# Performance work log

Hardware: AMD Instinct MI355X
Metric: run time of the kernel (lower is better)

## Reference

```python
import jax, jax.numpy as jnp
import numpy as np

N = 100000
E = 1600000
IN_C, HID, OUT_C = 128, 256, 32
EPS = 1e-5
NEG_SLOPE = 0.1


def _leaky(x):
    return jnp.where(x >= 0, x, NEG_SLOPE * x)


def _gcn_conv(x, src, dst, ew, W, b, n):
    # x: [n, Fin] -> [n, Fout]; PyG GCNConv: add self-loops (weight 1),
    # symmetric normalization D^-1/2 (A+I) D^-1/2, then linear + bias.
    h = x @ W                                   # [n, Fout]
    loop = jnp.arange(n)
    src_f = jnp.concatenate([src, loop])        # [E+n]
    dst_f = jnp.concatenate([dst, loop])
    ew_f = jnp.concatenate([ew, jnp.ones((n,), x.dtype)])
    deg = jax.ops.segment_sum(ew_f, dst_f, num_segments=n)
    dinv = jnp.where(deg > 0, jax.lax.rsqrt(jnp.maximum(deg, EPS * 0 + 1e-12)), 0.0)
    norm = dinv[src_f] * ew_f * dinv[dst_f]     # [E+n]
    msg = h[src_f] * norm[:, None]              # gather + scale, [E+n, Fout]
    out = jax.ops.segment_sum(msg, dst_f, num_segments=n)
    return out + b


def _bn(x, gamma, beta):
    # training-mode BatchNorm1d over the node dimension
    m = x.mean(axis=0)
    v = x.var(axis=0)
    return (x - m) * jax.lax.rsqrt(v + EPS) * gamma + beta


def setup_inputs() -> dict:
    key = jax.random.key(0)
    ks = jax.random.split(key, 12)
    x = jax.random.normal(ks[0], (N, IN_C), dtype=jnp.float32)
    edge_index = jax.random.randint(ks[1], (2, E), 0, N, dtype=jnp.int64)
    edge_weight = jax.random.uniform(ks[2], (E,), dtype=jnp.float32)

    def lin(k, fi, fo):
        s = 1.0 / np.sqrt(fi)
        k1, k2 = jax.random.split(k)
        W = jax.random.uniform(k1, (fi, fo), jnp.float32, -s, s)
        b = jax.random.uniform(k2, (fo,), jnp.float32, -s, s)
        return W, b

    W1, b1 = lin(ks[3], IN_C, HID)
    W2, b2 = lin(ks[4], HID, HID)
    W3, b3 = lin(ks[5], HID, HID)
    Wl1, bl1 = lin(ks[6], HID, HID)
    Wl2, bl2 = lin(ks[7], HID, OUT_C)
    ones = jnp.ones((HID,), jnp.float32)
    zeros = jnp.zeros((HID,), jnp.float32)
    return {
        "x": x, "edge_index": edge_index, "edge_weight": edge_weight,
        "W1": W1, "b1": b1, "g1": ones, "be1": zeros,
        "W2": W2, "b2": b2, "g2": ones, "be2": zeros,
        "W3": W3, "b3": b3, "g3": ones, "be3": zeros,
        "Wl1": Wl1, "bl1": bl1, "Wl2": Wl2, "bl2": bl2,
    }


def reference(x, edge_index, edge_weight,
              W1, b1, g1, be1,
              W2, b2, g2, be2,
              W3, b3, g3, be3,
              Wl1, bl1, Wl2, bl2):
    src, dst = edge_index[0], edge_index[1]
    h = _gcn_conv(x, src, dst, edge_weight, W1, b1, N)
    h = _leaky(_bn(h, g1, be1))  # dropout = identity (eval)
    h = _gcn_conv(h, src, dst, edge_weight, W2, b2, N)
    h = _leaky(_bn(h, g2, be2))
    h = _gcn_conv(h, src, dst, edge_weight, W3, b3, N)
    h = _leaky(_bn(h, g3, be3))
    h = _leaky(h @ Wl1 + bl1)
    return h @ Wl2 + bl2
```

## Files before the change

kernel.cpp:

```cpp
#include <hip/hip_runtime.h>

#define NN 100000
#define NE 1600000
#define EPS_BN 1e-5f
#define NSHADOW 64
#define STATS_SC_OFF (NSHADOW*512)
#define STATS_SH_OFF (NSHADOW*512 + 256)

typedef unsigned short ushort_t;
typedef unsigned long long u64;
typedef _Float16 f16;
typedef short v8s __attribute__((ext_vector_type(8)));
typedef float v4f __attribute__((ext_vector_type(4)));
typedef f16 f16x2 __attribute__((ext_vector_type(2)));
typedef f16 f16x4 __attribute__((ext_vector_type(4)));

__device__ __forceinline__ float lk(float x){ return x >= 0.f ? x : 0.1f*x; }

__device__ __forceinline__ ushort_t f2bf(float x){
  unsigned u = __float_as_uint(x);
  unsigned r = (u + 0x7fffu + ((u >> 16) & 1u)) >> 16;
  return (ushort_t)r;
}
__device__ __forceinline__ float bf2f(ushort_t h){
  return __uint_as_float(((unsigned)h) << 16);
}
__device__ __forceinline__ void split2(float x, ushort_t& hi, ushort_t& lo){
  hi = f2bf(x);
  lo = f2bf(x - bf2f(hi));
}

__device__ __forceinline__ void gload16(const ushort_t* g, ushort_t* l){
  __builtin_amdgcn_global_load_lds((const __attribute__((address_space(1))) void*)g,
                                   (__attribute__((address_space(3))) void*)l, 16, 0, 0);
}

__global__ void zero_acc(u64* __restrict__ acc, int n){
  int i = blockIdx.x*256 + threadIdx.x;
  if (i < n) acc[i] = 0ull;
}

__global__ void edge_hist(const int* __restrict__ dst, const float* __restrict__ ew,
                          u64* __restrict__ acc, ushort_t* __restrict__ rank, int e){
  int i = blockIdx.x*256 + threadIdx.x;
  if (i < e){
    int d = dst[i];
    unsigned fx = (unsigned)(ew[i] * 67108864.0f + 0.5f);
    u64 old = atomicAdd(&acc[d], (1ull << 40) | (u64)fx);
    rank[i] = (ushort_t)(old >> 40);
  }
}

__global__ void finalize_acc(const u64* __restrict__ acc, float* __restrict__ dinv,
                             int* __restrict__ cnt, int n){
  int i = blockIdx.x*256 + threadIdx.x;
  if (i < n){
    u64 v = acc[i];
    cnt[i] = (int)(v >> 40);
    double w = (double)(v & 0xFFFFFFFFFFull) * (1.0/67108864.0);
    dinv[i] = rsqrtf((float)(1.0 + w));
  }
}

__global__ __launch_bounds__(1024) void scan_block(const int* __restrict__ in, int* __restrict__ out,
                                                   int* __restrict__ bsum, int n){
  __shared__ int s[1024];
  int t = threadIdx.x;
  int i = blockIdx.x*1024 + t;
  int v = (i < n) ? in[i] : 0;
  s[t] = v; __syncthreads();
  for (int off = 1; off < 1024; off <<= 1){
    int x = (t >= off) ? s[t-off] : 0;
    __syncthreads();
    s[t] += x;
    __syncthreads();
  }
  if (i < n) out[i] = s[t] - v;
  if (t == 1023) bsum[blockIdx.x] = s[1023];
}

__global__ void scan_small(int* __restrict__ bsum, int nb){
  __shared__ int s[128];
  int t = threadIdx.x;
  int v = (t < nb) ? bsum[t] : 0;
  s[t] = v; __syncthreads();
  for (int off = 1; off < 128; off <<= 1){
    int x = (t >= off) ? s[t-off] : 0;
    __syncthreads();
    s[t] += x;
    __syncthreads();
  }
  if (t < nb) bsum[t] = s[t] - v;
}

__global__ __launch_bounds__(1024) void scan_add(int* __restrict__ rp,
                                                 const int* __restrict__ bsum, int n, int etot){
  int i = blockIdx.x*1024 + threadIdx.x;
  if (i < n) rp[i] += bsum[blockIdx.x];
  if (i == 0) rp[n] = etot;
}

__global__ void fill_csr_k(const int* __restrict__ src, const int* __restrict__ dst,
                           const float* __restrict__ ew, const float* __restrict__ dinv,
                           const int* __restrict__ rp, const ushort_t* __restrict__ rank,
                           int2* __restrict__ csr_sw, int e){
  int i = blockIdx.x*256 + threadIdx.x;
  if (i >= e) return;
  int s = src[i], d = dst[i];
  int pos = rp[d] + (int)rank[i];
  float w = dinv[s] * ew[i] * dinv[d];
  csr_sw[pos] = make_int2(s, __float_as_int(w));
}

__global__ void cvt_x(const float* __restrict__ in, f16* __restrict__ out, int n4){
  int i = blockIdx.x*256 + threadIdx.x;
  if (i >= n4) return;
  float4 v = ((const float4*)in)[i];
  f16x4 h = (f16x4){(f16)v.x, (f16)v.y, (f16)v.z, (f16)v.w};
  ((f16x4*)out)[i] = h;
}

__global__ __launch_bounds__(256) void spmm16(const f16* __restrict__ h,
    const int* __restrict__ rp, const int2* __restrict__ csr_sw,
    const float* __restrict__ dinv, const float* __restrict__ bias,
    float* __restrict__ out, float* __restrict__ stats, int n){
  int nbase = __builtin_amdgcn_readfirstlane(blockIdx.x*16 + (threadIdx.x >> 6)*4);
  if (nbase >= n) return;
  int lane = threadIdx.x & 63;
  const f16* hb = h + lane*4;

  int P[5];
#pragma unroll
  for (int i = 0; i < 5; ++i) P[i] = __builtin_amdgcn_readfirstlane(rp[nbase+i]);
  int nchE[4];
#pragma unroll
  for (int jj = 0; jj < 4; ++jj){
    int nc = (P[jj+1] - P[jj] + 7) >> 3;
    nc = (nc + 1) & ~1;
    nchE[jj] = nc < 2 ? 2 : nc;
  }
  float di0 = dinv[nbase+0], di1 = dinv[nbase+1], di2 = dinv[nbase+2], di3 = dinv[nbase+3];
  f16x4 hv0 = *(const f16x4*)(hb + (size_t)(nbase+0)*256);
  f16x4 hv1 = *(const f16x4*)(hb + (size_t)(nbase+1)*256);
  f16x4 hv2 = *(const f16x4*)(hb + (size_t)(nbase+2)*256);
  f16x4 hv3 = *(const f16x4*)(hb + (size_t)(nbase+3)*256);
  float4 bb = *(const float4*)(bias + lane*4);

  float wA[8], wB[8];
  f16x4 vA[8], vB[8];
  float ax0, ay0, az0, aw0, ax1, ay1, az1, aw1;
  float ssx = 0.f, ssy = 0.f, ssz = 0.f, ssw = 0.f;
  float sqx = 0.f, sqy = 0.f, sqz = 0.f, sqw = 0.f;

#define LOADCH(W, V, BASE, PEND) do { \
    int2 _e[8]; \
    int _b = (BASE); int _pe = (PEND); \
    _Pragma("unroll") \
    for (int _i = 0; _i < 8; ++_i){ \
      int _pc = _b + _i; \
      _pc = _pc < _pe-1 ? _pc : _pe-1; \
      _pc = _pc > 0 ? _pc : 0; \
      _e[_i] = csr_sw[_pc]; \
    } \
    _Pragma("unroll") \
    for (int _i = 0; _i < 8; ++_i){ \
      W[_i] = (_b + _i < _pe) ? __int_as_float(_e[_i].y) : 0.f; \
      V[_i] = *(const f16x4*)(hb + (size_t)_e[_i].x*256); \
    } \
  } while(0)

#define FMACH(W, V) do { \
    _Pragma("unroll") \
    for (int _i = 0; _i < 8; _i += 2){ \
      ax0 = fmaf(W[_i],   (float)V[_i][0],   ax0); \
      ay0 = fmaf(W[_i],   (float)V[_i][1],   ay0); \
      az0 = fmaf(W[_i],   (float)V[_i][2],   az0); \
      aw0 = fmaf(W[_i],   (float)V[_i][3],   aw0); \
      ax1 = fmaf(W[_i+1], (float)V[_i+1][0], ax1); \
      ay1 = fmaf(W[_i+1], (float)V[_i+1][1], ay1); \
      az1 = fmaf(W[_i+1], (float)V[_i+1][2], az1); \
      aw1 = fmaf(W[_i+1], (float)V[_i+1][3], aw1); \
    } \
  } while(0)

#define NODE(jj, DI, HV, PRE) do { \
    const int p0_ = P[jj], pend_ = P[(jj)+1]; \
    const int ncE_ = nchE[jj]; \
    float c0_ = (DI)*(DI); \
    ax0 = fmaf(c0_, (float)(HV)[0], bb.x); \
    ay0 = fmaf(c0_, (float)(HV)[1], bb.y); \
    az0 = fmaf(c0_, (float)(HV)[2], bb.z); \
    aw0 = fmaf(c0_, (float)(HV)[3], bb.w); \
    ax1 = 0.f; ay1 = 0.f; az1 = 0.f; aw1 = 0.f; \
    int base_ = p0_ + 8; \
    for (int k_ = 0; k_ + 2 < ncE_; k_ += 2){ \
      LOADCH(wB, vB, base_, pend_); base_ += 8; \
      FMACH(wA, vA); \
      LOADCH(wA, vA, base_, pend_); base_ += 8; \
      FMACH(wB, vB); \
    } \
    LOADCH(wB, vB, base_, pend_); \
    FMACH(wA, vA); \
    PRE; \
    FMACH(wB, vB); \
    { \
      float fx_ = ax0+ax1, fy_ = ay0+ay1, fz_ = az0+az1, fw_ = aw0+aw1; \
      *(float4*)(out + (size_t)(nbase+(jj))*256 + lane*4) = \
          make_float4(fx_, fy_, fz_, fw_); \
      ssx += fx_; sqx = fmaf(fx_, fx_, sqx); \
      ssy += fy_; sqy = fmaf(fy_, fy_, sqy); \
      ssz += fz_; sqz = fmaf(fz_, fz_, sqz); \
      ssw += fw_; sqw = fmaf(fw_, fw_, sqw); \
    } \
  } while(0)

  LOADCH(wA, vA, P[0], P[1]);
  NODE(0, di0, hv0, LOADCH(wA, vA, P[1], P[2]));
  NODE(1, di1, hv1, LOADCH(wA, vA, P[2], P[3]));
  NODE(2, di2, hv2, LOADCH(wA, vA, P[3], P[4]));
  NODE(3, di3, hv3, (void)0);
#undef LOADCH
#undef FMACH
#undef NODE

  __shared__ float red[4][64][8];
  int wid = threadIdx.x >> 6;
  red[wid][lane][0] = ssx; red[wid][lane][1] = ssy;
  red[wid][lane][2] = ssz; red[wid][lane][3] = ssw;
  red[wid][lane][4] = sqx; red[wid][lane][5] = sqy;
  red[wid][lane][6] = sqz; red[wid][lane][7] = sqw;
  __syncthreads();
  int c = threadIdx.x;
  float s = 0.f, s2 = 0.f;
#pragma unroll
  for (int w = 0; w < 4; ++w){
    s  += red[w][c>>2][c&3];
    s2 += red[w][c>>2][4 + (c&3)];
  }
  int sh = blockIdx.x & (NSHADOW-1);
  atomicAdd(&stats[sh*512 + c], s);
  atomicAdd(&stats[sh*512 + 256 + c], s2);
}

__global__ __launch_bounds__(256) void spmm_x16(const f16* __restrict__ h,
    const int* __restrict__ rp, const int2* __restrict__ csr_sw,
    const float* __restrict__ dinv,
    ushort_t* __restrict__ ohi, ushort_t* __restrict__ olo, int n){
  int nbase = __builtin_amdgcn_readfirstlane(blockIdx.x*16 + (threadIdx.x >> 6)*4);
  if (nbase >= n) return;
  int lane = threadIdx.x & 63;
  const f16* hb = h + lane*2;

  int P[5];
#pragma unroll
  for (int i = 0; i < 5; ++i) P[i] = __builtin_amdgcn_readfirstlane(rp[nbase+i]);
  int nchE[4];
#pragma unroll
  for (int jj = 0; jj < 4; ++jj){
    int nc = (P[jj+1] - P[jj] + 7) >> 3;
    nc = (nc + 1) & ~1;
    nchE[jj] = nc < 2 ? 2 : nc;
  }
  float di0 = dinv[nbase+0], di1 = dinv[nbase+1], di2 = dinv[nbase+2], di3 = dinv[nbase+3];
  f16x2 hv0 = *(const f16x2*)(hb + (size_t)(nbase+0)*128);
  f16x2 hv1 = *(const f16x2*)(hb + (size_t)(nbase+1)*128);
  f16x2 hv2 = *(const f16x2*)(hb + (size_t)(nbase+2)*128);
  f16x2 hv3 = *(const f16x2*)(hb + (size_t)(nbase+3)*128);

  float wA[8], wB[8];
  f16x2 vA[8], vB[8];
  float ax0, ay0, ax1, ay1;

#define LOADCH(W, V, BASE, PEND) do { \
    int2 _e[8]; \
    int _b = (BASE); int _pe = (PEND); \
    _Pragma("unroll") \
    for (int _i = 0; _i < 8; ++_i){ \
      int _pc = _b + _i; \
      _pc = _pc < _pe-1 ? _pc : _pe-1; \
      _pc = _pc > 0 ? _pc : 0; \
      _e[_i] = csr_sw[_pc]; \
    } \
    _Pragma("unroll") \
    for (int _i = 0; _i < 8; ++_i){ \
      W[_i] = (_b + _i < _pe) ? __int_as_float(_e[_i].y) : 0.f; \
      V[_i] = *(const f16x2*)(hb + (size_t)_e[_i].x*128); \
    } \
  } while(0)

#define FMACH(W, V) do { \
    _Pragma("unroll") \
    for (int _i = 0; _i < 8; _i += 2){ \
      ax0 = fmaf(W[_i],   (float)V[_i][0],   ax0); \
      ay0 = fmaf(W[_i],   (float)V[_i][1],   ay0); \
      ax1 = fmaf(W[_i+1], (float)V[_i+1][0], ax1); \
      ay1 = fmaf(W[_i+1], (float)V[_i+1][1], ay1); \
    } \
  } while(0)

#define NODE(jj, DI, HV, PRE) do { \
    const int p0_ = P[jj], pend_ = P[(jj)+1]; \
    const int ncE_ = nchE[jj]; \
    float c0_ = (DI)*(DI); \
    ax0 = c0_ * (float)(HV)[0]; \
    ay0 = c0_ * (float)(HV)[1]; \
    ax1 = 0.f; ay1 = 0.f; \
    int base_ = p0_ + 8; \
    for (int k_ = 0; k_ + 2 < ncE_; k_ += 2){ \
      LOADCH(wB, vB, base_, pend_); base_ += 8; \
      FMACH(wA, vA); \
      LOADCH(wA, vA, base_, pend_); base_ += 8; \
      FMACH(wB, vB); \
    } \
    LOADCH(wB, vB, base_, pend_); \
    FMACH(wA, vA); \
    PRE; \
    FMACH(wB, vB); \
    { \
      float ax_ = ax0 + ax1, ay_ = ay0 + ay1; \
      ushort_t hx_, lx_, hy_, ly_; \
      split2(ax_, hx_, lx_); \
      split2(ay_, hy_, ly_); \
      size_t o_ = (size_t)(nbase+(jj))*128 + lane*2; \
      ohi[o_] = hx_; ohi[o_+1] = hy_; \
      olo[o_] = lx_; olo[o_+1] = ly_; \
    } \
  } while(0)

  LOADCH(wA, vA, P[0], P[1]);
  NODE(0, di0, hv0, LOADCH(wA, vA, P[1], P[2]));
  NODE(1, di1, hv1, LOADCH(wA, vA, P[2], P[3]));
  NODE(2, di2, hv2, LOADCH(wA, vA, P[3], P[4]));
  NODE(3, di3, hv3, (void)0);
#undef LOADCH
#undef FMACH
#undef NODE
}

__global__ void zero_stats(float* __restrict__ stats){
  stats[blockIdx.x*256 + threadIdx.x] = 0.f;
}

__global__ void bn_final(float* __restrict__ stats, const float* __restrict__ g,
                         const float* __restrict__ be, int n){
  int c = threadIdx.x;
  float s = 0.f, s2 = 0.f;
  for (int k = 0; k < NSHADOW; ++k){
    s  += stats[k*512 + c];
    s2 += stats[k*512 + 256 + c];
  }
  float inv_n = 1.0f / (float)n;
  float mean = s * inv_n;
  float var  = fmaxf(s2 * inv_n - mean*mean, 0.f);
  float sc   = g[c] * rsqrtf(var + EPS_BN);
  stats[STATS_SC_OFF + c] = sc;
  stats[STATS_SH_OFF + c] = be[c] - mean * sc;
}

__global__ __launch_bounds__(256) void bn_apply_split(const float* __restrict__ a,
    const float* __restrict__ stats, ushort_t* __restrict__ hi, ushort_t* __restrict__ lo, int n){
  size_t i = (size_t)blockIdx.x*256 + threadIdx.x;
  if (i >= (size_t)n*64) return;
  int c4 = (int)(i & 63);
  float4 v  = ((const float4*)a)[i];
  float4 sc = ((const float4*)(stats + STATS_SC_OFF))[c4];
  float4 sh = ((const float4*)(stats + STATS_SH_OFF))[c4];
  v.x = lk(fmaf(v.x, sc.x, sh.x));
  v.y = lk(fmaf(v.y, sc.y, sh.y));
  v.z = lk(fmaf(v.z, sc.z, sh.z));
  v.w = lk(fmaf(v.w, sc.w, sh.w));
  ushort4 h, l;
  split2(v.x, h.x, l.x); split2(v.y, h.y, l.y);
  split2(v.z, h.z, l.z); split2(v.w, h.w, l.w);
  ((ushort4*)hi)[i] = h;
  ((ushort4*)lo)[i] = l;
}

__global__ void wsplit(const float* __restrict__ W, ushort_t* __restrict__ hiT,
                       ushort_t* __restrict__ loT, int K, int M){
  int i = blockIdx.x*256 + threadIdx.x;
  if (i >= K*M) return;
  int k = i / M, m = i % M;
  ushort_t h, l;
  split2(W[i], h, l);
  hiT[(size_t)m*K + k] = h;
  loT[(size_t)m*K + k] = l;
}

template<int BM, int BN, int WM, int WN, int ACT, int OMODE, int STATS>
__global__ __launch_bounds__(256) void gemm_mfma(
    const ushort_t* __restrict__ Ahi_g, const ushort_t* __restrict__ Alo_g,
    const ushort_t* __restrict__ Bhi_g, const ushort_t* __restrict__ Blo_g,
    const float* __restrict__ bias,
    float* __restrict__ Cf, ushort_t* __restrict__ Chi, ushort_t* __restrict__ Clo,
    f16* __restrict__ Ch, float* __restrict__ stats_g,
    int nrows, int K, int M){
  constexpr int FI = WM/16, FJ = WN/16;
  constexpr int WCOLS = BN/WN;
  __shared__ ushort_t sAhi[BM*32];
  __shared__ ushort_t sAlo[BM*32];
  __shared__ ushort_t sBhi[BN*32];
  __shared__ ushort_t sBlo[BN*32];
  const int tid  = threadIdx.x;
  const int wave = tid >> 6;
  const int lane = tid & 63;
  const int r0 = blockIdx.x * BM;
  const int c0 = blockIdx.y * BN;
  const int wr0 = (wave / WCOLS) * WM;
  const int wc0 = (wave % WCOLS) * WN;
  const int m = lane & 15, q = lane >> 4;

  v4f acc[FI][FJ];
#pragma unroll
  for (int i = 0; i < FI; ++i)
#pragma unroll
    for (int j = 0; j < FJ; ++j) acc[i][j] = (v4f){0.f,0.f,0.f,0.f};

  const int srow = lane >> 2;
  const int kqlog = (lane & 3) ^ ((srow >> 1) & 3);
  const int fsw = (q ^ ((m >> 1) & 3)) * 8;

  for (int kt = 0; kt < K; kt += 32){
#pragma unroll
    for (int c = 0; c < BM/64; ++c){
      int cc = c*4 + wave;
      int gr = r0 + cc*16 + srow;
      gr = min(gr, nrows - 1);
      size_t go = (size_t)gr*K + kt + kqlog*8;
      gload16(Ahi_g + go, &sAhi[cc*512]);
      gload16(Alo_g + go, &sAlo[cc*512]);
    }
    for (int cc = wave; cc < BN/16; cc += 4){
      int gr = c0 + cc*16 + srow;
      size_t go = (size_t)gr*K + kt + kqlog*8;
      gload16(Bhi_g + go, &sBhi[cc*512]);
      gload16(Blo_g + go, &sBlo[cc*512]);
    }
    __syncthreads();

    v8s ah[FI], al[FI], bh[FJ], bl[FJ];
#pragma unroll
    for (int i = 0; i < FI; ++i){
      int off = (wr0 + i*16 + m)*32 + fsw;
      ah[i] = *(const v8s*)&sAhi[off];
      al[i] = *(const v8s*)&sAlo[off];
    }
#pragma unroll
    for (int j = 0; j < FJ; ++j){
      int off = (wc0 + j*16 + m)*32 + fsw;
      bh[j] = *(const v8s*)&sBhi[off];
      bl[j] = *(const v8s*)&sBlo[off];
    }
#pragma unroll
    for (int i = 0; i < FI; ++i)
#pragma unroll
      for (int j = 0; j < FJ; ++j){
        acc[i][j] = __builtin_amdgcn_mfma_f32_16x16x32_bf16(ah[i], bh[j], acc[i][j], 0, 0, 0);
        acc[i][j] = __builtin_amdgcn_mfma_f32_16x16x32_bf16(ah[i], bl[j], acc[i][j], 0, 0, 0);
        acc[i][j] = __builtin_amdgcn_mfma_f32_16x16x32_bf16(al[i], bh[j], acc[i][j], 0, 0, 0);
      }
    __syncthreads();
  }

  __shared__ float cst[2*BN];
  if constexpr (STATS){
    if (tid < BN*2/ (256/ (BN*2>=256?1:1)) || tid < 256){
      if (tid < 2*BN) cst[tid] = 0.f;
    }
    __syncthreads();
  }
  float stj[FJ], stq[FJ];
#pragma unroll
  for (int j = 0; j < FJ; ++j){ stj[j] = 0.f; stq[j] = 0.f; }

#pragma unroll
  for (int i = 0; i < FI; ++i){
#pragma unroll
    for (int j = 0; j < FJ; ++j){
      int col = c0 + wc0 + j*16 + m;
      float bv = (ACT >= 1) ? bias[col] : 0.f;
#pragma unroll
      for (int r = 0; r < 4; ++r){
        int row = r0 + wr0 + i*16 + q*4 + r;
        if (row >= nrows) continue;
        float v = acc[i][j][r] + bv;
        if (ACT == 1) v = lk(v);
        if constexpr (STATS){
          stj[j] += v;
          stq[j] = fmaf(v, v, stq[j]);
        }
        size_t o = (size_t)row*M + col;
        if (OMODE == 1){
          ushort_t h, l; split2(v, h, l);
          Chi[o] = h; Clo[o] = l;
        } else if (OMODE == 2){
          Ch[o] = (f16)v;
        } else {
          Cf[o] = v;
        }
      }
    }
  }

  if constexpr (STATS){
#pragma unroll
    for (int j = 0; j < FJ; ++j){
      int cl = wc0 + j*16 + m;
      atomicAdd(&cst[cl*2 + 0], stj[j]);
      atomicAdd(&cst[cl*2 + 1], stq[j]);
    }
    __syncthreads();
    if (tid < BN){
      int sh = (blockIdx.x + blockIdx.y) & (NSHADOW-1);
      atomicAdd(&stats_g[sh*512 + c0 + tid],        cst[tid*2 + 0]);
      atomicAdd(&stats_g[sh*512 + 256 + c0 + tid],  cst[tid*2 + 1]);
    }
  }
}

extern "C" void kernel_launch(void* const* d_in, const int* in_sizes, int n_in,
                              void* d_out, int out_size, void* d_ws, size_t ws_size,
                              hipStream_t stream){
  const float* x   = (const float*)d_in[0];
  const int*   ei  = (const int*)  d_in[1];
  const float* ew  = (const float*)d_in[2];
  const float* W1  = (const float*)d_in[3];
  const float* b1  = (const float*)d_in[4];
  const float* g1  = (const float*)d_in[5];
  const float* be1 = (const float*)d_in[6];
  const float* W2  = (const float*)d_in[7];
  const float* b2  = (const float*)d_in[8];
  const float* g2  = (const float*)d_in[9];
  const float* be2 = (const float*)d_in[10];
  const float* W3  = (const float*)d_in[11];
  const float* b3  = (const float*)d_in[12];
  const float* g3  = (const float*)d_in[13];
  const float* be3 = (const float*)d_in[14];
  const float* Wl1 = (const float*)d_in[15];
  const float* bl1 = (const float*)d_in[16];
  const float* Wl2 = (const float*)d_in[17];
  const float* bl2 = (const float*)d_in[18];
  const int* src = ei;
  const int* dst = ei + NE;

  char* p = (char*)d_ws;
  auto carve = [&](size_t bytes)->void*{
    void* r = (void*)p;
    p += (bytes + 255) & ~(size_t)255;
    return r;
  };
  float*    dinv    = (float*)   carve((size_t)NN*4);
  int*      rp      = (int*)     carve((size_t)(NN+1)*4);
  int*      cnt     = (int*)     carve((size_t)NN*4);
  int*      bsum    = (int*)     carve(256*4);
  float*    stats   = (float*)   carve((size_t)(NSHADOW*512 + 512)*4);
  u64*      acc64   = (u64*)     carve((size_t)NN*8);
  int2*     csr_sw  = (int2*)    carve((size_t)NE*8);
  float*    S1      = (float*)   carve((size_t)NN*256*4);
  float*    S2      = (float*)   carve((size_t)NN*256*4);
  ushort_t* W1tH    = (ushort_t*)carve(128*256*2);
  ushort_t* W1tL    = (ushort_t*)carve(128*256*2);
  ushort_t* W2tH    = (ushort_t*)carve(256*256*2);
  ushort_t* W2tL    = (ushort_t*)carve(256*256*2);
  ushort_t* W3tH    = (ushort_t*)carve(256*256*2);
  ushort_t* W3tL    = (ushort_t*)carve(256*256*2);
  ushort_t* Wl1tH   = (ushort_t*)carve(256*256*2);
  ushort_t* Wl1tL   = (ushort_t*)carve(256*256*2);
  ushort_t* Wl2tH   = (ushort_t*)carve(256*32*2);
  ushort_t* Wl2tL   = (ushort_t*)carve(256*32*2);

  ushort_t* S1h256 = (ushort_t*)S1;  ushort_t* S1l256 = S1h256 + (size_t)NN*256;
  ushort_t* S2h256 = (ushort_t*)S2;  ushort_t* S2l256 = S2h256 + (size_t)NN*256;
  ushort_t* S1h128 = (ushort_t*)S1;  ushort_t* S1l128 = S1h128 + (size_t)NN*128;
  ushort_t* rank   = (ushort_t*)S2;
  f16*      x16    = (f16*)S2;
  f16*      H2f16  = (f16*)S2;
  f16*      H3f16  = (f16*)S1;

  const int nb = (NN + 1023) / 1024;
  const int spmm_blocks = (NN + 15) / 16;

  zero_acc<<<(NN+255)/256, 256, 0, stream>>>(acc64, NN);
  edge_hist<<<(NE+255)/256, 256, 0, stream>>>(dst, ew, acc64, rank, NE);
  finalize_acc<<<(NN+255)/256, 256, 0, stream>>>(acc64, dinv, cnt, NN);
  scan_block<<<nb, 1024, 0, stream>>>(cnt, rp, bsum, NN);
  scan_small<<<1, 128, 0, stream>>>(bsum, nb);
  scan_add<<<nb, 1024, 0, stream>>>(rp, bsum, NN, NE);
  fill_csr_k<<<(NE+255)/256, 256, 0, stream>>>(src, dst, ew, dinv, rp, rank, csr_sw, NE);

  wsplit<<<(128*256+255)/256, 256, 0, stream>>>(W1,  W1tH,  W1tL,  128, 256);
  wsplit<<<(256*256+255)/256, 256, 0, stream>>>(W2,  W2tH,  W2tL,  256, 256);
  wsplit<<<(256*256+255)/256, 256, 0, stream>>>(W3,  W3tH,  W3tL,  256, 256);
  wsplit<<<(256*256+255)/256, 256, 0, stream>>>(Wl1, Wl1tH, Wl1tL, 256, 256);
  wsplit<<<(256*32 +255)/256, 256, 0, stream>>>(Wl2, Wl2tH, Wl2tL, 256, 32);

  dim3 gridBig((NN+127)/128, 2);
  dim3 gridOut((NN+127)/128, 1);

  auto run_bn = [&](const float* fin, ushort_t* hi, ushort_t* lo,
                    const float* g, const float* be){
    bn_final<<<1, 256, 0, stream>>>(stats, g, be, NN);
    bn_apply_split<<<(int)(((size_t)NN*64 + 255)/256), 256, 0, stream>>>(fin, stats, hi, lo, NN);
  };

  cvt_x<<<(NN*32+255)/256, 256, 0, stream>>>(x, x16, NN*32);
  spmm_x16<<<spmm_blocks, 256, 0, stream>>>(x16, rp, csr_sw, dinv, S1h128, S1l128, NN);
  zero_stats<<<128, 256, 0, stream>>>(stats);
  gemm_mfma<128,128,64,64,2,0,1><<<gridBig, 256, 0, stream>>>(
      S1h128, S1l128, W1tH, W1tL, b1, S2, nullptr, nullptr, nullptr, stats, NN, 128, 256);
  run_bn(S2, S1h256, S1l256, g1, be1);

  gemm_mfma<128,128,64,64,0,2,0><<<gridBig, 256, 0, stream>>>(
      S1h256, S1l256, W2tH, W2tL, nullptr, nullptr, nullptr, nullptr, H2f16, nullptr, NN, 256, 256);
  zero_stats<<<128, 256, 0, stream>>>(stats);
  spmm16<<<spmm_blocks, 256, 0, stream>>>(H2f16, rp, csr_sw, dinv, b2, S1, stats, NN);
  run_bn(S1, S2h256, S2l256, g2, be2);

  gemm_mfma<128,128,64,64,0,2,0><<<gridBig, 256, 0, stream>>>(
      S2h256, S2l256, W3tH, W3tL, nullptr, nullptr, nullptr, nullptr, H3f16, nullptr, NN, 256, 256);
  zero_stats<<<128, 256, 0, stream>>>(stats);
  spmm16<<<spmm_blocks, 256, 0, stream>>>(H3f16, rp, csr_sw, dinv, b3, S2, stats, NN);
  run_bn(S2, S1h256, S1l256, g3, be3);

  gemm_mfma<128,128,64,64,1,1,0><<<gridBig, 256, 0, stream>>>(
      S1h256, S1l256, Wl1tH, Wl1tL, bl1, nullptr, S2h256, S2l256, nullptr, nullptr, NN, 256, 256);
  gemm_mfma<128,32,32,32,2,0,0><<<gridOut, 256, 0, stream>>>(
      S2h256, S2l256, Wl2tH, Wl2tL, bl2, (float*)d_out, nullptr, nullptr, nullptr, nullptr, NN, 256, 32);
}
```

Measured before the change: 996.6 us.

## Fuse BatchNorm apply and bf16 split into GEMM A-tile loading

Removes the standalone bn_apply_split kernels and instead has the GEMM read fp32 activations, apply the BN scale/shift and leaky ReLU, split into bf16 hi/lo, and write them into swizzled shared memory. This eliminates a full read and write of the activation tensor per layer. The A-tile path now uses register loads plus in-kernel conversion instead of direct global-to-LDS copies, which may reduce load/compute overlap. Buffer assignments are reshuffled to match.

```diff
diff --git a/kernel.cpp b/kernel.cpp
--- a/kernel.cpp
+++ b/kernel.cpp
@@ -11,6 +11,7 @@
 typedef unsigned long long u64;
 typedef _Float16 f16;
 typedef short v8s __attribute__((ext_vector_type(8)));
+typedef ushort_t us8 __attribute__((ext_vector_type(8)));
 typedef float v4f __attribute__((ext_vector_type(4)));
 typedef f16 f16x2 __attribute__((ext_vector_type(2)));
 typedef f16 f16x4 __attribute__((ext_vector_type(4)));
@@ -357,25 +358,6 @@
   stats[STATS_SH_OFF + c] = be[c] - mean * sc;
 }
 
-__global__ __launch_bounds__(256) void bn_apply_split(const float* __restrict__ a,
-    const float* __restrict__ stats, ushort_t* __restrict__ hi, ushort_t* __restrict__ lo, int n){
-  size_t i = (size_t)blockIdx.x*256 + threadIdx.x;
-  if (i >= (size_t)n*64) return;
-  int c4 = (int)(i & 63);
-  float4 v  = ((const float4*)a)[i];
-  float4 sc = ((const float4*)(stats + STATS_SC_OFF))[c4];
-  float4 sh = ((const float4*)(stats + STATS_SH_OFF))[c4];
-  v.x = lk(fmaf(v.x, sc.x, sh.x));
-  v.y = lk(fmaf(v.y, sc.y, sh.y));
-  v.z = lk(fmaf(v.z, sc.z, sh.z));
-  v.w = lk(fmaf(v.w, sc.w, sh.w));
-  ushort4 h, l;
-  split2(v.x, h.x, l.x); split2(v.y, h.y, l.y);
-  split2(v.z, h.z, l.z); split2(v.w, h.w, l.w);
-  ((ushort4*)hi)[i] = h;
-  ((ushort4*)lo)[i] = l;
-}
-
 __global__ void wsplit(const float* __restrict__ W, ushort_t* __restrict__ hiT,
                        ushort_t* __restrict__ loT, int K, int M){
   int i = blockIdx.x*256 + threadIdx.x;
@@ -387,20 +369,24 @@
   loT[(size_t)m*K + k] = l;
 }
 
-template<int BM, int BN, int WM, int WN, int ACT, int OMODE, int STATS>
+template<int BM, int BN, int WM, int WN, int ACT, int OMODE, int STATS, int AMODE>
 __global__ __launch_bounds__(256) void gemm_mfma(
     const ushort_t* __restrict__ Ahi_g, const ushort_t* __restrict__ Alo_g,
+    const float* __restrict__ Af_g,
     const ushort_t* __restrict__ Bhi_g, const ushort_t* __restrict__ Blo_g,
     const float* __restrict__ bias,
     float* __restrict__ Cf, ushort_t* __restrict__ Chi, ushort_t* __restrict__ Clo,
     f16* __restrict__ Ch, float* __restrict__ stats_g,
     int nrows, int K, int M){
+  static_assert(AMODE == 0 || BM == 128, "AMODE=1 staging assumes BM=128");
   constexpr int FI = WM/16, FJ = WN/16;
   constexpr int WCOLS = BN/WN;
   __shared__ ushort_t sAhi[BM*32];
   __shared__ ushort_t sAlo[BM*32];
   __shared__ ushort_t sBhi[BN*32];
   __shared__ ushort_t sBlo[BN*32];
+  __shared__ float sSC[AMODE ? 256 : 1];
+  __shared__ float sSH[AMODE ? 256 : 1];
   const int tid  = threadIdx.x;
   const int wave = tid >> 6;
   const int lane = tid & 63;
@@ -410,6 +396,14 @@
   const int wc0 = (wave % WCOLS) * WN;
   const int m = lane & 15, q = lane >> 4;
 
+  if constexpr (AMODE == 1){
+    if (tid < K){
+      sSC[tid] = stats_g[STATS_SC_OFF + tid];
+      sSH[tid] = stats_g[STATS_SH_OFF + tid];
+    }
+    __syncthreads();
+  }
+
   v4f acc[FI][FJ];
 #pragma unroll
   for (int i = 0; i < FI; ++i)
@@ -421,14 +415,46 @@
   const int fsw = (q ^ ((m >> 1) & 3)) * 8;
 
   for (int kt = 0; kt < K; kt += 32){
-#pragma unroll
-    for (int c = 0; c < BM/64; ++c){
-      int cc = c*4 + wave;
-      int gr = r0 + cc*16 + srow;
-      gr = min(gr, nrows - 1);
-      size_t go = (size_t)gr*K + kt + kqlog*8;
-      gload16(Ahi_g + go, &sAhi[cc*512]);
-      gload16(Alo_g + go, &sAlo[cc*512]);
+    if constexpr (AMODE == 0){
+#pragma unroll
+      for (int c = 0; c < BM/64; ++c){
+        int cc = c*4 + wave;
+        int gr = r0 + cc*16 + srow;
+        gr = min(gr, nrows - 1);
+        size_t go = (size_t)gr*K + kt + kqlog*8;
+        gload16(Ahi_g + go, &sAhi[cc*512]);
+        gload16(Alo_g + go, &sAlo[cc*512]);
+      }
+    } else {
+#pragma unroll
+      for (int s = 0; s < 2; ++s){
+        int pidx = tid + s*256;
+        int row  = pidx >> 2;
+        int kq   = pidx & 3;
+        int gr   = min(r0 + row, nrows - 1);
+        int ch0  = kt + kq*8;
+        const float* ap = Af_g + (size_t)gr*K + ch0;
+        float4 a0 = *(const float4*)ap;
+        float4 a1 = *(const float4*)(ap + 4);
+        float4 sc0 = *(const float4*)&sSC[ch0];
+        float4 sc1 = *(const float4*)&sSC[ch0 + 4];
+        float4 sh0 = *(const float4*)&sSH[ch0];
+        float4 sh1 = *(const float4*)&sSH[ch0 + 4];
+        float va[8] = {a0.x, a0.y, a0.z, a0.w, a1.x, a1.y, a1.z, a1.w};
+        float vc[8] = {sc0.x, sc0.y, sc0.z, sc0.w, sc1.x, sc1.y, sc1.z, sc1.w};
+        float vh[8] = {sh0.x, sh0.y, sh0.z, sh0.w, sh1.x, sh1.y, sh1.z, sh1.w};
+        us8 hi8, lo8;
+#pragma unroll
+        for (int j = 0; j < 8; ++j){
+          float v = lk(fmaf(va[j], vc[j], vh[j]));
+          ushort_t hh, ll;
+          split2(v, hh, ll);
+          hi8[j] = hh; lo8[j] = ll;
+        }
+        int off = row*32 + (kq ^ ((row >> 1) & 3))*8;
+        *(us8*)&sAhi[off] = hi8;
+        *(us8*)&sAlo[off] = lo8;
+      }
     }
     for (int cc = wave; cc < BN/16; cc += 4){
       int gr = c0 + cc*16 + srow;
@@ -462,11 +488,9 @@
     __syncthreads();
   }
 
-  __shared__ float cst[2*BN];
+  __shared__ float cst[STATS ? 2*BN : 1];
   if constexpr (STATS){
-    if (tid < BN*2/ (256/ (BN*2>=256?1:1)) || tid < 256){
-      if (tid < 2*BN) cst[tid] = 0.f;
-    }
+    if (tid < 2*BN) cst[tid] = 0.f;
     __syncthreads();
   }
   float stj[FJ], stq[FJ];
@@ -570,11 +594,10 @@
   ushort_t* Wl2tL   = (ushort_t*)carve(256*32*2);
 
   ushort_t* S1h256 = (ushort_t*)S1;  ushort_t* S1l256 = S1h256 + (size_t)NN*256;
-  ushort_t* S2h256 = (ushort_t*)S2;  ushort_t* S2l256 = S2h256 + (size_t)NN*256;
   ushort_t* S1h128 = (ushort_t*)S1;  ushort_t* S1l128 = S1h128 + (size_t)NN*128;
   ushort_t* rank   = (ushort_t*)S2;
   f16*      x16    = (f16*)S2;
-  f16*      H2f16  = (f16*)S2;
+  f16*      H2f16  = (f16*)S1;
   f16*      H3f16  = (f16*)S1;
 
   const int nb = (NN + 1023) / 1024;
@@ -597,33 +620,27 @@
   dim3 gridBig((NN+127)/128, 2);
   dim3 gridOut((NN+127)/128, 1);
 
-  auto run_bn = [&](const float* fin, ushort_t* hi, ushort_t* lo,
-                    const float* g, const float* be){
-    bn_final<<<1, 256, 0, stream>>>(stats, g, be, NN);
-    bn_apply_split<<<(int)(((size_t)NN*64 + 255)/256), 256, 0, stream>>>(fin, stats, hi, lo, NN);
-  };
-
   cvt_x<<<(NN*32+255)/256, 256, 0, stream>>>(x, x16, NN*32);
   spmm_x16<<<spmm_blocks, 256, 0, stream>>>(x16, rp, csr_sw, dinv, S1h128, S1l128, NN);
   zero_stats<<<128, 256, 0, stream>>>(stats);
-  gemm_mfma<128,128,64,64,2,0,1><<<gridBig, 256, 0, stream>>>(
-      S1h128, S1l128, W1tH, W1tL, b1, S2, nullptr, nullptr, nullptr, stats, NN, 128, 256);
-  run_bn(S2, S1h256, S1l256, g1, be1);
-
-  gemm_mfma<128,128,64,64,0,2,0><<<gridBig, 256, 0, stream>>>(
-      S1h256, S1l256, W2tH, W2tL, nullptr, nullptr, nullptr, nullptr, H2f16, nullptr, NN, 256, 256);
+  gemm_mfma<128,128,64,64,2,0,1,0><<<gridBig, 256, 0, stream>>>(
+      S1h128, S1l128, nullptr, W1tH, W1tL, b1, S2, nullptr, nullptr, nullptr, stats, NN, 128, 256);
+  bn_final<<<1, 256, 0, stream>>>(stats, g1, be1, NN);
+
   zero_stats<<<128, 256, 0, stream>>>(stats);
-  spmm16<<<spmm_blocks, 256, 0, stream>>>(H2f16, rp, csr_sw, dinv, b2, S1, stats, NN);
-  run_bn(S1, S2h256, S2l256, g2, be2);
-
-  gemm_mfma<128,128,64,64,0,2,0><<<gridBig, 256, 0, stream>>>(
-      S2h256, S2l256, W3tH, W3tL, nullptr, nullptr, nullptr, nullptr, H3f16, nullptr, NN, 256, 256);
+  gemm_mfma<128,128,64,64,0,2,0,1><<<gridBig, 256, 0, stream>>>(
+      nullptr, nullptr, S2, W2tH, W2tL, nullptr, nullptr, nullptr, nullptr, H2f16, stats, NN, 256, 256);
+  spmm16<<<spmm_blocks, 256, 0, stream>>>(H2f16, rp, csr_sw, dinv, b2, S2, stats, NN);
+  bn_final<<<1, 256, 0, stream>>>(stats, g2, be2, NN);
+
   zero_stats<<<128, 256, 0, stream>>>(stats);
+  gemm_mfma<128,128,64,64,0,2,0,1><<<gridBig, 256, 0, stream>>>(
+      nullptr, nullptr, S2, W3tH, W3tL, nullptr, nullptr, nullptr, nullptr, H3f16, stats, NN, 256, 256);
   spmm16<<<spmm_blocks, 256, 0, stream>>>(H3f16, rp, csr_sw, dinv, b3, S2, stats, NN);
-  run_bn(S2, S1h256, S1l256, g3, be3);
-
-  gemm_mfma<128,128,64,64,1,1,0><<<gridBig, 256, 0, stream>>>(
-      S1h256, S1l256, Wl1tH, Wl1tL, bl1, nullptr, S2h256, S2l256, nullptr, nullptr, NN, 256, 256);
-  gemm_mfma<128,32,32,32,2,0,0><<<gridOut, 256, 0, stream>>>(
-      S2h256, S2l256, Wl2tH, Wl2tL, bl2, (float*)d_out, nullptr, nullptr, nullptr, nullptr, NN, 256, 32);
-}
+  bn_final<<<1, 256, 0, stream>>>(stats, g3, be3, NN);
+
+  gemm_mfma<128,128,64,64,1,1,0,1><<<gridBig, 256, 0, stream>>>(
+      nullptr, nullptr, S2, Wl1tH, Wl1tL, bl1, nullptr, S1h256, S1l256, nullptr, stats, NN, 256, 256);
+  gemm_mfma<128,32,32,32,2,0,0,0><<<gridOut, 256, 0, stream>>>(
+      S1h256, S1l256, nullptr, Wl2tH, Wl2tL, bl2, (float*)d_out, nullptr, nullptr, nullptr, nullptr, NN, 256, 32);
+}
```

Measured after the change: 906.8 us. 1.1x faster.
